# Kernel tuning notes

Hardware: AMD Instinct MI355X
Metric: run time of the kernel (lower is better)

Reference implementation:

```python
import jax, jax.numpy as jnp
import numpy as np

MIN_N, MAX_N = 3, 5
ALPHA = 5  # 'ATCGN'
VOCAB = sum(ALPHA ** n for n in range(MIN_N, MAX_N + 1))  # 3875


def setup_inputs() -> dict:
    key = jax.random.key(0)
    k1, _ = jax.random.split(key)
    B, S = 4096, 512
    tokens = jax.random.randint(k1, (B, S), 0, ALPHA, dtype=jnp.int32)
    n_grams = sum(S - n + 1 for n in range(MIN_N, MAX_N + 1))  # 3S-9
    values = jnp.ones((B, n_grams), dtype=jnp.float32)
    return {"tokens": tokens, "values": values}


def _ngram_indices(tokens):
    """Exact arithmetic replacement of the StaticHashTable lookup.

    vocab index of an n-gram c0..c_{n-1} = offset_n + sum_i c_i * 5^{n-1-i},
    matching itertools.product('ATCGN', repeat=n) enumeration order.
    """
    B, S = tokens.shape
    idx_list = []
    offset = 0
    for n in range(MIN_N, MAX_N + 1):
        W = S - n + 1  # number of windows
        idx = jnp.zeros((B, W), dtype=jnp.int32)
        for i in range(n):
            idx = idx + tokens[:, i:W + i] * (ALPHA ** (n - 1 - i))
        idx_list.append(idx + offset)
        offset += ALPHA ** n
    return jnp.concatenate(idx_list, axis=1)  # [B, 3S-9]


def reference(tokens, values):
    B = tokens.shape[0]
    idx = _ngram_indices(tokens)                       # [B, G] in [0, VOCAB)
    rows = jnp.arange(B, dtype=jnp.int32)[:, None]     # [B, 1] broadcast over G
    # binary presence histogram: max-scatter of the ones payload (dedup is
    # implicit, matching tf.unique + binary SparseTensor -> dense)
    out = jnp.zeros((B, VOCAB), dtype=jnp.float32).at[rows, idx].max(values)
    return out
```

## Files before the change

### kernel.cpp

```cpp
#include <hip/hip_runtime.h>


#define VOCAB 3875
#define SEQ   512
#define G3    (SEQ - 2)
#define G4    (SEQ - 3)
#define G5    (SEQ - 4)
#define OFF4  125
#define OFF5  750
#define NT    512
#define BMW   122

__global__ __launch_bounds__(NT) void ngram_bitmap_kernel(
        const int* __restrict__ tokens,
        float* __restrict__ out) {
    __shared__ int tok[SEQ];
    __shared__ unsigned int bm[BMW];

    const int b   = blockIdx.x;
    const int tid = threadIdx.x;

    const int myTok = tokens[(size_t)b * SEQ + tid];
    if (tid < BMW) bm[tid] = 0u;
    tok[tid] = myTok;
    __syncthreads();

    if (tid < G3) {
        const int r3 = myTok * 25 + tok[tid + 1] * 5 + tok[tid + 2];
        atomicOr(&bm[r3 >> 5], 1u << (r3 & 31));
        if (tid < G4) {
            const int r4 = r3 * 5 + tok[tid + 3];
            const int v4 = OFF4 + r4;
            atomicOr(&bm[v4 >> 5], 1u << (v4 & 31));
            if (tid < G5) {
                const int v5 = OFF5 + r4 * 5 + tok[tid + 4];
                atomicOr(&bm[v5 >> 5], 1u << (v5 & 31));
            }
        }
    }
    __syncthreads();

    float* orow = out + (size_t)b * VOCAB;
    #pragma unroll
    for (int i = tid; i < VOCAB; i += NT) {
        const unsigned int w = bm[i >> 5];
        orow[i] = ((w >> (i & 31)) & 1u) ? 1.0f : 0.0f;
    }
}

extern "C" void kernel_launch(void* const* d_in, const int* in_sizes, int n_in,
                              void* d_out, int out_size, void* d_ws, size_t ws_size,
                              hipStream_t stream) {
    const int* tokens = (const int*)d_in[0];
    float*     out    = (float*)d_out;

    const int B = in_sizes[0] / SEQ;
    ngram_bitmap_kernel<<<B, NT, 0, stream>>>(tokens, out);
}
```

Measured before the change: 92.79 us.

## Process four rows per block with vectorized int4 loads and float4 stores

Each block now handles four batch rows instead of one. Tokens are loaded as int4 and output is written as 16-byte float4 stores across the contiguous 4-row span. This targets store-bandwidth inefficiency from scalar, misaligned row writes (VOCAB is odd) and cuts block count to a quarter. It adds integer division per element and assumes B is divisible by 4.

```diff
diff --git a/kernel.cpp b/kernel.cpp
--- a/kernel.cpp
+++ b/kernel.cpp
@@ -9,42 +9,59 @@
 #define OFF4  125
 #define OFF5  750
 #define NT    512
-#define BMW   122
+#define RPB   4
+#define BMS   128
 
-__global__ __launch_bounds__(NT) void ngram_bitmap_kernel(
+typedef float floatx4 __attribute__((ext_vector_type(4)));
+
+__global__ __launch_bounds__(NT) void ngram_bitmap4_kernel(
         const int* __restrict__ tokens,
         float* __restrict__ out) {
-    __shared__ int tok[SEQ];
-    __shared__ unsigned int bm[BMW];
+    __shared__ __align__(16) int tok[RPB * SEQ];
+    __shared__ unsigned int bm[RPB * BMS];
 
     const int b   = blockIdx.x;
     const int tid = threadIdx.x;
 
-    const int myTok = tokens[(size_t)b * SEQ + tid];
-    if (tid < BMW) bm[tid] = 0u;
-    tok[tid] = myTok;
+    const int4* tsrc = (const int4*)(tokens + (size_t)b * (RPB * SEQ));
+    ((int4*)tok)[tid] = tsrc[tid];
+    bm[tid] = 0u;
     __syncthreads();
 
-    if (tid < G3) {
-        const int r3 = myTok * 25 + tok[tid + 1] * 5 + tok[tid + 2];
-        atomicOr(&bm[r3 >> 5], 1u << (r3 & 31));
-        if (tid < G4) {
-            const int r4 = r3 * 5 + tok[tid + 3];
-            const int v4 = OFF4 + r4;
-            atomicOr(&bm[v4 >> 5], 1u << (v4 & 31));
-            if (tid < G5) {
-                const int v5 = OFF5 + r4 * 5 + tok[tid + 4];
-                atomicOr(&bm[v5 >> 5], 1u << (v5 & 31));
+    {
+        const int row  = tid >> 7;
+        const int lane = tid & 127;
+        const int* tr = tok + row * SEQ;
+        unsigned int* bmr = bm + row * BMS;
+        for (int i = lane; i < G3; i += 128) {
+            const int r3 = tr[i] * 25 + tr[i + 1] * 5 + tr[i + 2];
+            atomicOr(&bmr[r3 >> 5], 1u << (r3 & 31));
+            if (i < G4) {
+                const int r4 = r3 * 5 + tr[i + 3];
+                const int v4 = OFF4 + r4;
+                atomicOr(&bmr[v4 >> 5], 1u << (v4 & 31));
+                if (i < G5) {
+                    const int v5 = OFF5 + r4 * 5 + tr[i + 4];
+                    atomicOr(&bmr[v5 >> 5], 1u << (v5 & 31));
+                }
             }
         }
     }
     __syncthreads();
 
-    float* orow = out + (size_t)b * VOCAB;
-    #pragma unroll
-    for (int i = tid; i < VOCAB; i += NT) {
-        const unsigned int w = bm[i >> 5];
-        orow[i] = ((w >> (i & 31)) & 1u) ? 1.0f : 0.0f;
+    floatx4* ov = (floatx4*)(out + (size_t)b * (RPB * VOCAB));
+    #pragma unroll 2
+    for (int v = tid; v < VOCAB; v += NT) {
+        floatx4 f;
+        #pragma unroll
+        for (int j = 0; j < 4; ++j) {
+            const int d = 4 * v + j;
+            const int r = d / VOCAB;
+            const int c = d - r * VOCAB;
+            const unsigned int w = bm[r * BMS + (c >> 5)];
+            f[j] = (float)((w >> (c & 31)) & 1u);
+        }
+        ov[v] = f;
     }
 }
 
@@ -55,5 +72,5 @@
     float*     out    = (float*)d_out;
 
     const int B = in_sizes[0] / SEQ;
-    ngram_bitmap_kernel<<<B, NT, 0, stream>>>(tokens, out);
+    ngram_bitmap4_kernel<<<B / RPB, NT, 0, stream>>>(tokens, out);
 }
```

After: 90.44 us (median of 2 runs). 1.03x faster.
